# Performance work log

Hardware: AMD Instinct MI355X
Metric: run time of the kernel (lower is better)

## Reference

```python
import jax, jax.numpy as jnp
from jax import lax
import numpy as np

# Dims: batch, input channels (=3*C), output channels, kernel size, spatial
B, CIN, C, K, H, W = 8, 576, 192, 3, 56, 56
KK = K * K  # number of kernel positions


def setup_inputs() -> dict:
    key = jax.random.key(0)
    k1, k2, k3, k4 = jax.random.split(key, 4)
    x = jax.random.normal(k1, (B, CIN, H, W), jnp.float32)
    # 1x1 conv producing per-channel, per-position dynamic logits (C*KK outputs)
    fc_w = jax.random.normal(k2, (C * KK, CIN), jnp.float32) * 0.05
    # per-position grouped conv kernels: (KK, C_out, CIN//C=3, K, K)
    w1 = jax.random.normal(k3, (KK, C, CIN // C, K, K), jnp.float32) * 0.1
    # per-position depthwise conv kernels: (KK, C, K, K)
    w2 = jax.random.normal(k4, (KK, C, K, K), jnp.float32) * 0.1
    return {"x": x, "fc_w": fc_w, "w1": w1, "w2": w2}


def reference(x, fc_w, w1, w2):
    b = x.shape[0]
    # dynamic softmax weights over the KK kernel positions: (b, C, KK, H, W)
    logits = jnp.einsum('oc,bchw->bohw', fc_w, x).reshape(b, C, KK, H, W)
    attn = jax.nn.softmax(logits, axis=2)

    # dep_conv1: per-position grouped conv (3C -> C, groups=C), vmapped over KK
    def conv1(wi):  # wi: (C, 3, K, K)
        return lax.conv_general_dilated(x, wi, (1, 1), 'SAME',
                                        feature_group_count=C)

    feat = jax.nn.relu(jax.vmap(conv1)(w1))  # (KK, b, C, H, W)

    # dep_conv2: per-position depthwise conv (C -> C, groups=C)
    def conv2(fi, wi):  # fi: (b, C, H, W), wi: (C, K, K)
        return lax.conv_general_dilated(fi, wi[:, None], (1, 1), 'SAME',
                                        feature_group_count=C)

    out_pos = jax.vmap(conv2)(feat, w2)  # (KK, b, C, H, W)

    # softmax-weighted aggregation over kernel positions
    out = jnp.einsum('ibchw,bcihw->bchw', out_pos, attn)  # (b, C, H, W)
    return out
```

## Files before the change

### kernel.cpp

```cpp
#include <hip/hip_runtime.h>
#include <hip/hip_bf16.h>

constexpr int Bn   = 8;
constexpr int Cin  = 576;
constexpr int Cc   = 192;
constexpr int Hh   = 56;
constexpr int Ww   = 56;
constexpr int HWn  = Hh * Ww;
constexpr int CKK  = Cc * 9;

constexpr int GM = 1792;
constexpr int GK = 576;
constexpr int GN = Bn * HWn;
constexpr int NKSTEP = GK / 32;

using f16x8 = __attribute__((ext_vector_type(8))) _Float16;
using f32x4 = __attribute__((ext_vector_type(4))) float;

__device__ __forceinline__ void async_copy16(void* lds, const void* gptr) {
    __builtin_amdgcn_global_load_lds(
        (const __attribute__((address_space(1))) unsigned int*)gptr,
        (__attribute__((address_space(3))) unsigned int*)lds, 16, 0, 0);
}

__device__ __forceinline__ float blo(unsigned int u) { return __uint_as_float(u << 16); }
__device__ __forceinline__ float bhi(unsigned int u) { return __uint_as_float(u & 0xffff0000u); }
__device__ __forceinline__ unsigned short bf16bits(float f) {
    union { __hip_bfloat16 h; unsigned short u; } c; c.h = __float2bfloat16(f); return c.u;
}

__global__ __launch_bounds__(256) void cast_fcw_kernel(
    const float* __restrict__ fcw, _Float16* __restrict__ out)
{
    int idx = blockIdx.x * 256 + threadIdx.x;
    int e = idx * 4;
    if (e >= GM * GK) return;
    int row = e / GK;
    union { ushort4 u; _Float16 h[4]; } pk;
    if (row < CKK) {
        float4 v = *(const float4*)&fcw[e];
        pk.h[0] = (_Float16)v.x; pk.h[1] = (_Float16)v.y;
        pk.h[2] = (_Float16)v.z; pk.h[3] = (_Float16)v.w;
    } else {
        pk.h[0] = pk.h[1] = pk.h[2] = pk.h[3] = (_Float16)0.f;
    }
    *(ushort4*)&out[e] = pk.u;
}

__global__ __launch_bounds__(256) void transpose_cast_kernel(
    const float* __restrict__ x, _Float16* __restrict__ xt)
{
    __shared__ float t[32][65];
    const int b = blockIdx.z, k0 = blockIdx.y * 32, hw0 = blockIdx.x * 64;
    const int tid = threadIdx.x;
    const int col = tid & 63, kr = tid >> 6;
#pragma unroll
    for (int p = 0; p < 8; p++) {
        int k = kr + p * 4;
        t[k][col] = x[(size_t)(b * Cin + k0 + k) * HWn + hw0 + col];
    }
    __syncthreads();
    const int row = tid >> 2, cq = (tid & 3) * 8;
    union { uint4 u; _Float16 h[8]; } pk;
#pragma unroll
    for (int j = 0; j < 8; j++) pk.h[j] = (_Float16)t[cq + j][row];
    *(uint4*)&xt[(size_t)(b * HWn + hw0 + row) * GK + k0 + cq] = pk.u;
}

__global__ __launch_bounds__(256, 2) void gemm_mfma_kernel(
    const _Float16* __restrict__ A, const _Float16* __restrict__ Bm,
    __hip_bfloat16* __restrict__ logits)
{
    const int lin = blockIdx.x;
    const int g = lin & 7, s = lin >> 3;
    const int mt = s % 7, nt = (s / 7) * 8 + g;
    if (nt >= 196) return;

    __shared__ _Float16 As[2][256 * 32];
    __shared__ _Float16 Bs[2][128 * 32];

    const int tid = threadIdx.x;
    const int n0 = nt * 128;
    const int m0 = mt * 256;
    const int lane = tid & 63;
    const int wave = tid >> 6;
    const int wm = (wave >> 1) * 128;
    const int wn = (wave & 1) * 64;
    const int lm = lane & 15;
    const int lc = lane >> 4;

    const int lrow = tid >> 2;
    const int koff = (((tid & 3) ^ ((tid >> 3) & 3)) << 3);

    int offA[8], offB[4];
#pragma unroll
    for (int i = 0; i < 8; i++) {
        int ra = wm + i * 16 + lm;
        offA[i] = ra * 32 + ((lc ^ ((ra >> 1) & 3)) << 3);
    }
#pragma unroll
    for (int j = 0; j < 4; j++) {
        int rb = wn + j * 16 + lm;
        offB[j] = rb * 32 + ((lc ^ ((rb >> 1) & 3)) << 3);
    }

    const _Float16* pA = A  + (size_t)(m0 + lrow) * GK + koff;
    const _Float16* pB = Bm + (size_t)(n0 + lrow) * GK + koff;

#define STAGE(buf, kk)                                                         \
    do {                                                                       \
        async_copy16(&As[buf][(size_t)tid * 8],        pA + (kk));             \
        async_copy16(&As[buf][2048  + (size_t)tid * 8], pA +  64 * GK + (kk)); \
        async_copy16(&As[buf][4096  + (size_t)tid * 8], pA + 128 * GK + (kk)); \
        async_copy16(&As[buf][6144  + (size_t)tid * 8], pA + 192 * GK + (kk)); \
        async_copy16(&Bs[buf][(size_t)tid * 8],        pB + (kk));             \
        async_copy16(&Bs[buf][2048  + (size_t)tid * 8], pB +  64 * GK + (kk)); \
    } while (0)

    STAGE(0, 0);
    STAGE(1, 32);
    asm volatile("s_waitcnt vmcnt(6)" ::: "memory");

    f32x4 acc[8][4] = {};

    for (int t = 0; t < NKSTEP; ++t) {
        const int cur = t & 1;
        __builtin_amdgcn_s_barrier();
        asm volatile("" ::: "memory");

        const _Float16* Ab = &As[cur][0];
        const _Float16* Bb = &Bs[cur][0];
        f16x8 bf[4];
#pragma unroll
        for (int j = 0; j < 4; j++) bf[j] = *(const f16x8*)&Bb[offB[j]];
#pragma unroll
        for (int i = 0; i < 8; i++) {
            f16x8 a = *(const f16x8*)&Ab[offA[i]];
#pragma unroll
            for (int j = 0; j < 4; j++)
                acc[i][j] = __builtin_amdgcn_mfma_f32_16x16x32_f16(bf[j], a, acc[i][j], 0, 0, 0);
        }

        asm volatile("" ::: "memory");
        __builtin_amdgcn_s_barrier();

        if (t + 2 < NKSTEP) {
            STAGE(cur, (t + 2) * 32);
            asm volatile("s_waitcnt vmcnt(6)" ::: "memory");
        } else {
            asm volatile("s_waitcnt vmcnt(0)" ::: "memory");
        }
    }
#undef STAGE

    const int mcol = m0 + wm + lm;
#pragma unroll
    for (int i = 0; i < 8; i++) {
        int m = mcol + i * 16;
        if (m >= CKK) continue;
#pragma unroll
        for (int j = 0; j < 4; j++) {
            int n = n0 + wn + j * 16 + lc * 4;
            int b = n / HWn, hw = n - b * HWn;
            uint2 pk;
            pk.x = (unsigned)bf16bits(acc[i][j][0]) | ((unsigned)bf16bits(acc[i][j][1]) << 16);
            pk.y = (unsigned)bf16bits(acc[i][j][2]) | ((unsigned)bf16bits(acc[i][j][3]) << 16);
            *(uint2*)&logits[((size_t)b * CKK + m) * HWn + hw] = pk;
        }
    }
}

__global__ __launch_bounds__(256, 4) void conv_fused_kernel(
    const float* __restrict__ x, const float* __restrict__ w1,
    const __hip_bfloat16* __restrict__ logits,
    const float* __restrict__ w2, float* __restrict__ out)
{
    const int c = blockIdx.x, hb = blockIdx.y, b = blockIdx.z;
    const int tid = threadIdx.x;
    const int h0 = hb * 14;

    __shared__ float xt[3][18][61];
    __shared__ unsigned short ft[9][16][72];

    for (int idx = tid; idx < 756; idx += 256) {
        int d = idx / 252, rem = idx - d * 252;
        int r = rem / 14, g = rem - r * 14;
        int h = h0 - 2 + r;
        float4 v = {0.f, 0.f, 0.f, 0.f};
        if (h >= 0 && h < Hh)
            v = *(const float4*)&x[((size_t)(b * Cin + 3 * c + d) * Hh + h) * Ww + 4 * g];
        xt[d][r][1 + 4 * g + 0] = v.x;
        xt[d][r][1 + 4 * g + 1] = v.y;
        xt[d][r][1 + 4 * g + 2] = v.z;
        xt[d][r][1 + 4 * g + 3] = v.w;
    }
    for (int idx = tid; idx < 108; idx += 256) {
        int d = idx / 36, rem = idx - d * 36;
        int r = rem >> 1, col = (rem & 1) ? 57 : 0;
        xt[d][r][col] = 0.f;
    }
    for (int idx = tid; idx < 288; idx += 256) {
        int i = idx / 32, rem = idx - i * 32;
        int r = rem >> 1, side = rem & 1;
        *(unsigned int*)&ft[i][r][side ? 58 : 0] = 0u;
    }

    const bool p2 = tid < 196;
    const int row2 = tid / 14, seg2 = tid - row2 * 14;
    const int hw2 = (h0 + row2) * Ww + 4 * seg2;

    __syncthreads();

    if (tid < 224) {
        const int row = tid / 14, seg = tid - (tid / 14) * 14;
        const int w0 = 4 * seg;
        const int fh = h0 - 1 + row;
        const bool valid = (fh >= 0) && (fh < Hh);

        float acc[9][4] = {};

#pragma unroll 1
        for (int d = 0; d < 3; d++) {
            float win[3][6];
#pragma unroll
            for (int u = 0; u < 3; u++)
#pragma unroll
                for (int k = 0; k < 6; k++)
                    win[u][k] = xt[d][row + u][w0 + k];

            const float* wb = w1 + (size_t)c * 27 + d * 9;
#pragma unroll
            for (int i = 0; i < 9; i++) {
                const float* wp = wb + (size_t)i * Cc * 27;
                float wgt[9];
#pragma unroll
                for (int j = 0; j < 9; j++) wgt[j] = wp[j];
#pragma unroll
                for (int u = 0; u < 3; u++)
#pragma unroll
                    for (int v = 0; v < 3; v++) {
                        float wv = wgt[u * 3 + v];
#pragma unroll
                        for (int p = 0; p < 4; p++)
                            acc[i][p] += win[u][p + v] * wv;
                    }
            }
        }

#pragma unroll
        for (int i = 0; i < 9; i++) {
            unsigned pk0 = 0u, pk1 = 0u;
            if (valid) {
                pk0 = (unsigned)bf16bits(fmaxf(acc[i][0], 0.f)) |
                      ((unsigned)bf16bits(fmaxf(acc[i][1], 0.f)) << 16);
                pk1 = (unsigned)bf16bits(fmaxf(acc[i][2], 0.f)) |
                      ((unsigned)bf16bits(fmaxf(acc[i][3], 0.f)) << 16);
            }
            unsigned int* dst = (unsigned int*)&ft[i][row][2 + w0];
            dst[0] = pk0; dst[1] = pk1;
        }
    }

    uint2 lv[9];
    if (p2) {
        const __hip_bfloat16* lbase = logits + ((size_t)b * CKK + c * 9) * HWn + hw2;
#pragma unroll
        for (int i = 0; i < 9; i++) lv[i] = *(const uint2*)&lbase[(size_t)i * HWn];
    }
    __syncthreads();

    if (p2) {
        const int w0 = 4 * seg2;

        float lg[9][4];
#pragma unroll
        for (int i = 0; i < 9; i++) {
            lg[i][0] = blo(lv[i].x); lg[i][1] = bhi(lv[i].x);
            lg[i][2] = blo(lv[i].y); lg[i][3] = bhi(lv[i].y);
        }
#pragma unroll
        for (int p = 0; p < 4; p++) {
            float mx = lg[0][p];
#pragma unroll
            for (int i = 1; i < 9; i++) mx = fmaxf(mx, lg[i][p]);
            float sum = 0.f;
#pragma unroll
            for (int i = 0; i < 9; i++) { lg[i][p] = __expf(lg[i][p] - mx); sum += lg[i][p]; }
            float inv = __builtin_amdgcn_rcpf(sum);
#pragma unroll
            for (int i = 0; i < 9; i++) lg[i][p] *= inv;
        }

        float oacc[4] = {};
#pragma unroll
        for (int i = 0; i < 9; i++) {
            const float* wp = w2 + ((size_t)i * Cc + c) * 9;
            float wgt[9];
#pragma unroll
            for (int j = 0; j < 9; j++) wgt[j] = wp[j];
            float cacc[4] = {};
#pragma unroll
            for (int u = 0; u < 3; u++) {
                const unsigned short* fr = &ft[i][row2 + u][w0];
                uint2 a = *(const uint2*)fr;
                uint2 b2 = *(const uint2*)(fr + 4);
                float wf[8];
                wf[0] = blo(a.x);  wf[1] = bhi(a.x);
                wf[2] = blo(a.y);  wf[3] = bhi(a.y);
                wf[4] = blo(b2.x); wf[5] = bhi(b2.x);
                wf[6] = blo(b2.y); wf[7] = bhi(b2.y);
#pragma unroll
                for (int v = 0; v < 3; v++) {
                    float wv = wgt[u * 3 + v];
#pragma unroll
                    for (int p = 0; p < 4; p++)
                        cacc[p] += wf[p + v + 1] * wv;
                }
            }
#pragma unroll
            for (int p = 0; p < 4; p++) oacc[p] += cacc[p] * lg[i][p];
        }

        float4 o;
        o.x = oacc[0]; o.y = oacc[1]; o.z = oacc[2]; o.w = oacc[3];
        *(float4*)&out[((size_t)(b * Cc + c)) * HWn + hw2] = o;
    }
}

extern "C" void kernel_launch(void* const* d_in, const int* in_sizes, int n_in,
                              void* d_out, int out_size, void* d_ws, size_t ws_size,
                              hipStream_t stream)
{
    const float* x    = (const float*)d_in[0];
    const float* fc_w = (const float*)d_in[1];
    const float* w1   = (const float*)d_in[2];
    const float* w2   = (const float*)d_in[3];
    float* out = (float*)d_out;

    char* ws = (char*)d_ws;
    __hip_bfloat16* logits = (__hip_bfloat16*)ws;
    _Float16* xt    = (_Float16*)(ws + (size_t)Bn * CKK * HWn * 2);
    _Float16* fcw16 = (_Float16*)(ws + (size_t)Bn * CKK * HWn * 2 + (size_t)GN * GK * 2);

    cast_fcw_kernel<<<(GM * GK / 4 + 255) / 256, 256, 0, stream>>>(fc_w, fcw16);
    transpose_cast_kernel<<<dim3(HWn / 64, GK / 32, Bn), 256, 0, stream>>>(x, xt);
    gemm_mfma_kernel<<<8 * 25 * 7, 256, 0, stream>>>(fcw16, xt, logits);
    conv_fused_kernel<<<dim3(Cc, 4, Bn), 256, 0, stream>>>(x, w1, logits, w2, out);
}
```

Baseline: 249.2 us.

## Fuse x transpose-cast into GEMM B-tile loading via register staging

Removes the separate transpose_cast kernel and its fp16 xt workspace. The GEMM now reads fp32 x directly from NCHW layout, converts it to fp16 in registers and writes swizzled B tiles into LDS, prefetching one k-step ahead while A still uses async global-to-LDS copies. This saves a kernel launch and a full write and re-read of the transposed activation. In exchange the GEMM issues strided, non-async scalar loads, which raises register pressure and may stall the MFMA loop. It also pads an LDS array in the conv kernel.

```diff
diff --git a/kernel.cpp b/kernel.cpp
--- a/kernel.cpp
+++ b/kernel.cpp
@@ -47,28 +47,8 @@
     *(ushort4*)&out[e] = pk.u;
 }
 
-__global__ __launch_bounds__(256) void transpose_cast_kernel(
-    const float* __restrict__ x, _Float16* __restrict__ xt)
-{
-    __shared__ float t[32][65];
-    const int b = blockIdx.z, k0 = blockIdx.y * 32, hw0 = blockIdx.x * 64;
-    const int tid = threadIdx.x;
-    const int col = tid & 63, kr = tid >> 6;
-#pragma unroll
-    for (int p = 0; p < 8; p++) {
-        int k = kr + p * 4;
-        t[k][col] = x[(size_t)(b * Cin + k0 + k) * HWn + hw0 + col];
-    }
-    __syncthreads();
-    const int row = tid >> 2, cq = (tid & 3) * 8;
-    union { uint4 u; _Float16 h[8]; } pk;
-#pragma unroll
-    for (int j = 0; j < 8; j++) pk.h[j] = (_Float16)t[cq + j][row];
-    *(uint4*)&xt[(size_t)(b * HWn + hw0 + row) * GK + k0 + cq] = pk.u;
-}
-
 __global__ __launch_bounds__(256, 2) void gemm_mfma_kernel(
-    const _Float16* __restrict__ A, const _Float16* __restrict__ Bm,
+    const _Float16* __restrict__ A, const float* __restrict__ X,
     __hip_bfloat16* __restrict__ logits)
 {
     const int lin = blockIdx.x;
@@ -104,22 +84,48 @@
         offB[j] = rb * 32 + ((lc ^ ((rb >> 1) & 3)) << 3);
     }
 
-    const _Float16* pA = A  + (size_t)(m0 + lrow) * GK + koff;
-    const _Float16* pB = Bm + (size_t)(n0 + lrow) * GK + koff;
-
-#define STAGE(buf, kk)                                                         \
+    const _Float16* pA = A + (size_t)(m0 + lrow) * GK + koff;
+
+    const int n_loc = tid & 127;
+    const int kh = tid >> 7;
+    const int n_glob = n0 + n_loc;
+    const int bb = n_glob / HWn;
+    const int hw = n_glob - bb * HWn;
+    const float* pxB = X + (size_t)(bb * Cin + kh * 16) * HWn + hw;
+
+    const int swz = (n_loc >> 1) & 3;
+    const int wrB0 = n_loc * 32 + ((2 * kh) ^ swz) * 8;
+    const int wrB1 = n_loc * 32 + ((2 * kh + 1) ^ swz) * 8;
+
+#define AGLDS(buf, kk)                                                         \
     do {                                                                       \
-        async_copy16(&As[buf][(size_t)tid * 8],        pA + (kk));             \
+        async_copy16(&As[buf][(size_t)tid * 8],         pA + (kk));            \
         async_copy16(&As[buf][2048  + (size_t)tid * 8], pA +  64 * GK + (kk)); \
         async_copy16(&As[buf][4096  + (size_t)tid * 8], pA + 128 * GK + (kk)); \
         async_copy16(&As[buf][6144  + (size_t)tid * 8], pA + 192 * GK + (kk)); \
-        async_copy16(&Bs[buf][(size_t)tid * 8],        pB + (kk));             \
-        async_copy16(&Bs[buf][2048  + (size_t)tid * 8], pB +  64 * GK + (kk)); \
     } while (0)
 
-    STAGE(0, 0);
-    STAGE(1, 32);
-    asm volatile("s_waitcnt vmcnt(6)" ::: "memory");
+#define BWRITE(buf, bv)                                                        \
+    do {                                                                       \
+        union { f16x8 v; _Float16 h[8]; } lo_, hi_;                            \
+        _Pragma("unroll")                                                      \
+        for (int j_ = 0; j_ < 8; j_++) {                                       \
+            lo_.h[j_] = (_Float16)(bv)[j_];                                    \
+            hi_.h[j_] = (_Float16)(bv)[8 + j_];                                \
+        }                                                                      \
+        *(f16x8*)&Bs[buf][wrB0] = lo_.v;                                       \
+        *(f16x8*)&Bs[buf][wrB1] = hi_.v;                                       \
+    } while (0)
+
+    float bv0[16];
+#pragma unroll
+    for (int j = 0; j < 16; j++) bv0[j] = pxB[j * HWn];
+    AGLDS(0, 0);
+    AGLDS(1, 32);
+    asm volatile("s_waitcnt vmcnt(8)" ::: "memory");
+    BWRITE(0, bv0);
+    asm volatile("s_waitcnt vmcnt(4)" ::: "memory");
+    asm volatile("s_waitcnt lgkmcnt(0)" ::: "memory");
 
     f32x4 acc[8][4] = {};
 
@@ -128,6 +134,13 @@
         __builtin_amdgcn_s_barrier();
         asm volatile("" ::: "memory");
 
+        float bv[16];
+        if (t + 1 < NKSTEP) {
+            const float* p = pxB + (size_t)(t + 1) * 32 * HWn;
+#pragma unroll
+            for (int j = 0; j < 16; j++) bv[j] = p[j * HWn];
+        }
+
         const _Float16* Ab = &As[cur][0];
         const _Float16* Bb = &Bs[cur][0];
         f16x8 bf[4];
@@ -144,14 +157,18 @@
         asm volatile("" ::: "memory");
         __builtin_amdgcn_s_barrier();
 
-        if (t + 2 < NKSTEP) {
-            STAGE(cur, (t + 2) * 32);
-            asm volatile("s_waitcnt vmcnt(6)" ::: "memory");
-        } else {
-            asm volatile("s_waitcnt vmcnt(0)" ::: "memory");
-        }
-    }
-#undef STAGE
+        if (t + 2 < NKSTEP) AGLDS(cur, (t + 2) * 32);
+        if (t + 1 < NKSTEP) {
+            if (t + 2 < NKSTEP)
+                asm volatile("s_waitcnt vmcnt(4)" ::: "memory");
+            else
+                asm volatile("s_waitcnt vmcnt(0)" ::: "memory");
+            BWRITE(cur ^ 1, bv);
+            asm volatile("s_waitcnt lgkmcnt(0)" ::: "memory");
+        }
+    }
+#undef AGLDS
+#undef BWRITE
 
     const int mcol = m0 + wm + lm;
 #pragma unroll
@@ -161,11 +178,11 @@
 #pragma unroll
         for (int j = 0; j < 4; j++) {
             int n = n0 + wn + j * 16 + lc * 4;
-            int b = n / HWn, hw = n - b * HWn;
+            int b = n / HWn, hw2 = n - b * HWn;
             uint2 pk;
             pk.x = (unsigned)bf16bits(acc[i][j][0]) | ((unsigned)bf16bits(acc[i][j][1]) << 16);
             pk.y = (unsigned)bf16bits(acc[i][j][2]) | ((unsigned)bf16bits(acc[i][j][3]) << 16);
-            *(uint2*)&logits[((size_t)b * CKK + m) * HWn + hw] = pk;
+            *(uint2*)&logits[((size_t)b * CKK + m) * HWn + hw2] = pk;
         }
     }
 }
@@ -179,7 +196,7 @@
     const int tid = threadIdx.x;
     const int h0 = hb * 14;
 
-    __shared__ float xt[3][18][61];
+    __shared__ float xt[3][18][65];
     __shared__ unsigned short ft[9][16][72];
 
     for (int idx = tid; idx < 756; idx += 256) {
@@ -339,11 +356,9 @@
 
     char* ws = (char*)d_ws;
     __hip_bfloat16* logits = (__hip_bfloat16*)ws;
-    _Float16* xt    = (_Float16*)(ws + (size_t)Bn * CKK * HWn * 2);
-    _Float16* fcw16 = (_Float16*)(ws + (size_t)Bn * CKK * HWn * 2 + (size_t)GN * GK * 2);
+    _Float16* fcw16 = (_Float16*)(ws + (size_t)Bn * CKK * HWn * 2);
 
     cast_fcw_kernel<<<(GM * GK / 4 + 255) / 256, 256, 0, stream>>>(fc_w, fcw16);
-    transpose_cast_kernel<<<dim3(HWn / 64, GK / 32, Bn), 256, 0, stream>>>(x, xt);
-    gemm_mfma_kernel<<<8 * 25 * 7, 256, 0, stream>>>(fcw16, xt, logits);
+    gemm_mfma_kernel<<<8 * 25 * 7, 256, 0, stream>>>(fcw16, x, logits);
     conv_fused_kernel<<<dim3(Cc, 4, Bn), 256, 0, stream>>>(x, w1, logits, w2, out);
 }
```

Measured after the change: 259.8 us. 1.04x slower.

## Load GEMM B operand directly to registers, double-buffered, bypassing LDS

Applied to the files above, without the earlier changes.

The MFMA GEMM no longer stages the B (activation) tile through LDS. Each wave loads its B fragments straight from global memory into registers, double-buffered across k-steps, while A keeps its async global-to-LDS pipeline with adjusted vmcnt waits. This cuts LDS traffic and footprint, at the cost of more registers and B rows being fetched redundantly by both wave rows. The conv kernel also pads its x tile row stride from 61 to 65 and drops two unused bf16 unpacks.

```diff
diff --git a/kernel.cpp b/kernel.cpp
--- a/kernel.cpp
+++ b/kernel.cpp
@@ -77,7 +77,6 @@
     if (nt >= 196) return;
 
     __shared__ _Float16 As[2][256 * 32];
-    __shared__ _Float16 Bs[2][128 * 32];
 
     const int tid = threadIdx.x;
     const int n0 = nt * 128;
@@ -92,66 +91,74 @@
     const int lrow = tid >> 2;
     const int koff = (((tid & 3) ^ ((tid >> 3) & 3)) << 3);
 
-    int offA[8], offB[4];
+    int offA[8];
 #pragma unroll
     for (int i = 0; i < 8; i++) {
         int ra = wm + i * 16 + lm;
         offA[i] = ra * 32 + ((lc ^ ((ra >> 1) & 3)) << 3);
     }
-#pragma unroll
-    for (int j = 0; j < 4; j++) {
-        int rb = wn + j * 16 + lm;
-        offB[j] = rb * 32 + ((lc ^ ((rb >> 1) & 3)) << 3);
-    }
-
-    const _Float16* pA = A  + (size_t)(m0 + lrow) * GK + koff;
-    const _Float16* pB = Bm + (size_t)(n0 + lrow) * GK + koff;
-
-#define STAGE(buf, kk)                                                         \
+
+    const _Float16* pA = A + (size_t)(m0 + lrow) * GK + koff;
+    const _Float16* pB0 = Bm + (size_t)(n0 + wn + lm) * GK + lc * 8;
+
+#define AGLDS(buf, kk)                                                         \
     do {                                                                       \
-        async_copy16(&As[buf][(size_t)tid * 8],        pA + (kk));             \
+        async_copy16(&As[buf][(size_t)tid * 8],         pA + (kk));            \
         async_copy16(&As[buf][2048  + (size_t)tid * 8], pA +  64 * GK + (kk)); \
         async_copy16(&As[buf][4096  + (size_t)tid * 8], pA + 128 * GK + (kk)); \
         async_copy16(&As[buf][6144  + (size_t)tid * 8], pA + 192 * GK + (kk)); \
-        async_copy16(&Bs[buf][(size_t)tid * 8],        pB + (kk));             \
-        async_copy16(&Bs[buf][2048  + (size_t)tid * 8], pB +  64 * GK + (kk)); \
     } while (0)
 
-    STAGE(0, 0);
-    STAGE(1, 32);
-    asm volatile("s_waitcnt vmcnt(6)" ::: "memory");
+#define BLOAD(dst, t1)                                                         \
+    do {                                                                       \
+        const _Float16* p_ = pB0 + (size_t)(t1) * 32;                          \
+        dst[0] = *(const f16x8*)(p_);                                          \
+        dst[1] = *(const f16x8*)(p_ + 16 * GK);                                \
+        dst[2] = *(const f16x8*)(p_ + 32 * GK);                                \
+        dst[3] = *(const f16x8*)(p_ + 48 * GK);                                \
+    } while (0)
+
+    f16x8 bfA[4], bfB[4];
+
+    BLOAD(bfA, 0);
+    asm volatile("" ::: "memory");
+    AGLDS(0, 0);
+    AGLDS(1, 32);
+    asm volatile("s_waitcnt vmcnt(4)" ::: "memory");
 
     f32x4 acc[8][4] = {};
 
-    for (int t = 0; t < NKSTEP; ++t) {
-        const int cur = t & 1;
-        __builtin_amdgcn_s_barrier();
-        asm volatile("" ::: "memory");
-
-        const _Float16* Ab = &As[cur][0];
-        const _Float16* Bb = &Bs[cur][0];
-        f16x8 bf[4];
-#pragma unroll
-        for (int j = 0; j < 4; j++) bf[j] = *(const f16x8*)&Bb[offB[j]];
-#pragma unroll
-        for (int i = 0; i < 8; i++) {
-            f16x8 a = *(const f16x8*)&Ab[offA[i]];
-#pragma unroll
-            for (int j = 0; j < 4; j++)
-                acc[i][j] = __builtin_amdgcn_mfma_f32_16x16x32_f16(bf[j], a, acc[i][j], 0, 0, 0);
-        }
-
-        asm volatile("" ::: "memory");
-        __builtin_amdgcn_s_barrier();
-
-        if (t + 2 < NKSTEP) {
-            STAGE(cur, (t + 2) * 32);
-            asm volatile("s_waitcnt vmcnt(6)" ::: "memory");
-        } else {
-            asm volatile("s_waitcnt vmcnt(0)" ::: "memory");
-        }
-    }
-#undef STAGE
+#define KSTEP(t, cur, bfC, bfN)                                                \
+    do {                                                                       \
+        if ((t) + 1 < NKSTEP) BLOAD(bfN, (t) + 1);                             \
+        __builtin_amdgcn_s_barrier();                                          \
+        asm volatile("" ::: "memory");                                         \
+        const _Float16* Ab = &As[cur][0];                                      \
+        _Pragma("unroll")                                                      \
+        for (int i = 0; i < 8; i++) {                                          \
+            f16x8 a = *(const f16x8*)&Ab[offA[i]];                             \
+            _Pragma("unroll")                                                  \
+            for (int j = 0; j < 4; j++)                                        \
+                acc[i][j] = __builtin_amdgcn_mfma_f32_16x16x32_f16(            \
+                    bfC[j], a, acc[i][j], 0, 0, 0);                            \
+        }                                                                      \
+        asm volatile("" ::: "memory");                                         \
+        __builtin_amdgcn_s_barrier();                                          \
+        if ((t) + 2 < NKSTEP) {                                                \
+            AGLDS(cur, ((t) + 2) * 32);                                        \
+            asm volatile("s_waitcnt vmcnt(8)" ::: "memory");                   \
+        } else if ((t) + 1 < NKSTEP) {                                         \
+            asm volatile("s_waitcnt vmcnt(4)" ::: "memory");                   \
+        }                                                                      \
+    } while (0)
+
+    for (int tt = 0; tt < NKSTEP; tt += 2) {
+        KSTEP(tt,     0, bfA, bfB);
+        KSTEP(tt + 1, 1, bfB, bfA);
+    }
+#undef KSTEP
+#undef AGLDS
+#undef BLOAD
 
     const int mcol = m0 + wm + lm;
 #pragma unroll
@@ -161,11 +168,11 @@
 #pragma unroll
         for (int j = 0; j < 4; j++) {
             int n = n0 + wn + j * 16 + lc * 4;
-            int b = n / HWn, hw = n - b * HWn;
+            int b = n / HWn, hw2 = n - b * HWn;
             uint2 pk;
             pk.x = (unsigned)bf16bits(acc[i][j][0]) | ((unsigned)bf16bits(acc[i][j][1]) << 16);
             pk.y = (unsigned)bf16bits(acc[i][j][2]) | ((unsigned)bf16bits(acc[i][j][3]) << 16);
-            *(uint2*)&logits[((size_t)b * CKK + m) * HWn + hw] = pk;
+            *(uint2*)&logits[((size_t)b * CKK + m) * HWn + hw2] = pk;
         }
     }
 }
@@ -179,7 +186,7 @@
     const int tid = threadIdx.x;
     const int h0 = hb * 14;
 
-    __shared__ float xt[3][18][61];
+    __shared__ float xt[3][18][65];
     __shared__ unsigned short ft[9][16][72];
 
     for (int idx = tid; idx < 756; idx += 256) {
@@ -305,10 +312,10 @@
                 uint2 a = *(const uint2*)fr;
                 uint2 b2 = *(const uint2*)(fr + 4);
                 float wf[8];
-                wf[0] = blo(a.x);  wf[1] = bhi(a.x);
+                wf[1] = bhi(a.x);
                 wf[2] = blo(a.y);  wf[3] = bhi(a.y);
                 wf[4] = blo(b2.x); wf[5] = bhi(b2.x);
-                wf[6] = blo(b2.y); wf[7] = bhi(b2.y);
+                wf[6] = blo(b2.y);
 #pragma unroll
                 for (int v = 0; v < 3; v++) {
                     float wv = wgt[u * 3 + v];
```

Result: slower. 274.3 us (+10.1%).
